# Kernel optimization log

Measured on AMD Instinct MI355X. Metric: run time of the kernel, lower is better.

## Reference

```python
import jax, jax.numpy as jnp
import numpy as np

QUERY_DIM = 512
INNER_DIM = 2 * QUERY_DIM  # 1024
CROSS_DIM = 512


def setup_inputs() -> dict:
    key = jax.random.key(0)
    k1, k2, k3, k4, k5, k6, k7 = jax.random.split(key, 7)
    B, N1, N2 = 8, 2048, 2048
    S1 = jax.random.normal(k1, (B, N1, CROSS_DIM), dtype=jnp.float32)
    S2 = jax.random.normal(k2, (B, N2, QUERY_DIM), dtype=jnp.float32)
    # Linear weights stored as [in, out] (pre-transposed vs torch's [out, in])
    sq = 1.0 / np.sqrt(QUERY_DIM)
    sc = 1.0 / np.sqrt(CROSS_DIM)
    si = 1.0 / np.sqrt(INNER_DIM)
    Wq = jax.random.uniform(k3, (QUERY_DIM, INNER_DIM), jnp.float32, -sq, sq)
    Wk = jax.random.uniform(k4, (CROSS_DIM, INNER_DIM), jnp.float32, -sc, sc)
    Wv = jax.random.uniform(k5, (CROSS_DIM, INNER_DIM), jnp.float32, -sc, sc)
    Wo = jax.random.uniform(k6, (INNER_DIM, QUERY_DIM), jnp.float32, -si, si)
    bo = jax.random.uniform(k7, (QUERY_DIM,), jnp.float32, -si, si)
    return {"S1": S1, "S2": S2, "Wq": Wq, "Wk": Wk, "Wv": Wv, "Wo": Wo, "bo": bo}


def reference(S1, S2, Wq, Wk, Wv, Wo, bo):
    # softmax((Wq S2)(Wk S1)^T) (Wv S1), then output projection. NOTE: no 1/sqrt(d) scaling.
    query = jnp.einsum('bnd,de->bne', S2, Wq)   # [B, N2, inner]
    key_ = jnp.einsum('bmd,de->bme', S1, Wk)    # [B, N1, inner]
    value = jnp.einsum('bmd,de->bme', S1, Wv)   # [B, N1, inner]
    scores = jnp.einsum('bne,bme->bnm', query, key_)  # [B, N2, N1]
    attn = jax.nn.softmax(scores, axis=-1)
    masked = jnp.einsum('bnm,bme->bne', attn, value)  # [B, N2, inner]
    out = jnp.einsum('bne,ed->bnd', masked, Wo) + bo  # [B, N2, query_dim]
    return out
```

## Files before the change

kernel.cpp:

```cpp
#include <hip/hip_runtime.h>


typedef _Float16 h_t;
typedef _Float16 h8 __attribute__((ext_vector_type(8)));
typedef _Float16 h4 __attribute__((ext_vector_type(4)));
typedef float f4 __attribute__((ext_vector_type(4)));

#define MFMA16(a, b, c) __builtin_amdgcn_mfma_f32_16x16x32_f16(a, b, c, 0, 0, 0)

typedef const __attribute__((address_space(1))) void* gas_t;
typedef __attribute__((address_space(3))) void* las_t;

__device__ __forceinline__ void gl2lds16(const void* g, void* l) {
    __builtin_amdgcn_global_load_lds((gas_t)g, (las_t)l, 16, 0, 0);
}

__global__ __launch_bounds__(256) void k_cast5(const float* __restrict__ S1,
                                               const float* __restrict__ S2,
                                               const float* __restrict__ Wq,
                                               const float* __restrict__ Wk,
                                               const float* __restrict__ Wv,
                                               h_t* __restrict__ S1h,
                                               h_t* __restrict__ S2h,
                                               h_t* __restrict__ Wqh,
                                               h_t* __restrict__ Wkh,
                                               h_t* __restrict__ Wvh) {
    long i = (long)blockIdx.x * 256 + threadIdx.x;
    const long n = 2097152;
    const long wn = 131072;
    const float* src;
    h_t* dst;
    long off;
    if (i < n) { src = S1; dst = S1h; off = i; }
    else if (i < 2 * n) { src = S2; dst = S2h; off = i - n; }
    else if (i < 2 * n + wn) { src = Wq; dst = Wqh; off = i - 2 * n; }
    else if (i < 2 * n + 2 * wn) { src = Wk; dst = Wkh; off = i - 2 * n - wn; }
    else { src = Wv; dst = Wvh; off = i - 2 * n - 2 * wn; }
    float4 v = *((const float4*)src + off);
    h4 h = {(h_t)v.x, (h_t)v.y, (h_t)v.z, (h_t)v.w};
    *((h4*)dst + off) = h;
}

__global__ __launch_bounds__(256) void k_transpose_o(const float* __restrict__ Wo,
                                                     h_t* __restrict__ Wot) {
    const int K = 1024, N = 512;
    int kb = blockIdx.y * 32, nb = blockIdx.x * 32;
    __shared__ float tile[32][33];
    int x = threadIdx.x & 31, y = threadIdx.x >> 5;
#pragma unroll
    for (int j = 0; j < 4; j++)
        tile[y + j * 8][x] = Wo[(size_t)(kb + y + j * 8) * N + nb + x];
    __syncthreads();
#pragma unroll
    for (int j = 0; j < 4; j++)
        Wot[(size_t)(nb + y + j * 8) * K + kb + x] = (h_t)tile[x][y + j * 8];
}

__global__ __launch_bounds__(256) void k_wpre(const h_t* __restrict__ Wqh,
                                              const h_t* __restrict__ Wkh,
                                              const h_t* __restrict__ Wot,
                                              const h_t* __restrict__ Wvh,
                                              h_t* __restrict__ Wkq,
                                              h_t* __restrict__ Wvot) {
    __shared__ h_t As[128 * 64];
    __shared__ h_t Bs[128 * 64];
    int t = threadIdx.x, w = t >> 6, lane = t & 63;
    int q16 = lane >> 4, l16 = lane & 15;
    int id = blockIdx.x;
    const h_t* A;
    const h_t* Bt;
    h_t* C;
    float oscale;
    if (id < 16) { A = Wkh; Bt = Wqh; C = Wkq; oscale = 1.44269504f; }
    else { id -= 16; A = Wot; Bt = Wvh; C = Wvot; oscale = 1.0f; }
    size_t m0 = (size_t)(id >> 2) * 128, n0 = (size_t)(id & 3) * 128;
    const int K = 1024, N = 512;
    int wr = (w >> 1) * 64, wc = (w & 1) * 64;
    f4 acc[4][4] = {};

    for (int k0 = 0; k0 < K; k0 += 64) {
#pragma unroll
        for (int j = 0; j < 4; j++) {
            int q = w * 4 + j;
            int row = q * 8 + (lane >> 3);
            int ks = (((lane & 7) ^ (row & 7)) << 3);
            gl2lds16(A + (m0 + row) * K + k0 + ks, &As[q * 512]);
            gl2lds16(Bt + (n0 + row) * K + k0 + ks, &Bs[q * 512]);
        }
        __syncthreads();
#pragma unroll
        for (int ks = 0; ks < 2; ks++) {
            h8 av[4], bv[4];
#pragma unroll
            for (int i = 0; i < 4; i++) {
                int row = wr + i * 16 + l16;
                int ch = ks * 4 + q16;
                av[i] = *(const h8*)&As[row * 64 + ((ch ^ (row & 7)) << 3)];
            }
#pragma unroll
            for (int j = 0; j < 4; j++) {
                int row = wc + j * 16 + l16;
                int ch = ks * 4 + q16;
                bv[j] = *(const h8*)&Bs[row * 64 + ((ch ^ (row & 7)) << 3)];
            }
#pragma unroll
            for (int i = 0; i < 4; i++)
#pragma unroll
                for (int j = 0; j < 4; j++)
                    acc[i][j] = MFMA16(av[i], bv[j], acc[i][j]);
        }
        __syncthreads();
    }
#pragma unroll
    for (int i = 0; i < 4; i++) {
        size_t r0 = m0 + wr + i * 16 + q16 * 4;
#pragma unroll
        for (int j = 0; j < 4; j++) {
            size_t c = n0 + wc + j * 16 + l16;
#pragma unroll
            for (int r = 0; r < 4; r++)
                C[(r0 + r) * N + c] = (h_t)(acc[i][j][r] * oscale);
        }
    }
}

__global__ __launch_bounds__(256) void k_proj2(const h_t* __restrict__ S2h,
                                               const h_t* __restrict__ S1h,
                                               const h_t* __restrict__ Wkq,
                                               const h_t* __restrict__ Wvot,
                                               const float* __restrict__ bo,
                                               h_t* __restrict__ T,
                                               h_t* __restrict__ Vt) {
    __shared__ h_t As[128 * 64];
    __shared__ h_t Bs[128 * 64];
    int t = threadIdx.x, w = t >> 6, lane = t & 63;
    int q16 = lane >> 4, l16 = lane & 15;
    int id = blockIdx.x;
    int mode = id >> 9;
    id &= 511;
    const h_t* A = mode ? S1h : S2h;
    const h_t* Bt = mode ? Wvot : Wkq;
    size_t m0 = (size_t)(id >> 2) * 128, n0 = (size_t)(id & 3) * 128;
    const int K = 512;
    int wr = (w >> 1) * 64, wc = (w & 1) * 64;
    f4 acc[4][4] = {};

    for (int k0 = 0; k0 < K; k0 += 64) {
#pragma unroll
        for (int j = 0; j < 4; j++) {
            int q = w * 4 + j;
            int row = q * 8 + (lane >> 3);
            int ks = (((lane & 7) ^ (row & 7)) << 3);
            gl2lds16(A + (m0 + row) * K + k0 + ks, &As[q * 512]);
            gl2lds16(Bt + (n0 + row) * K + k0 + ks, &Bs[q * 512]);
        }
        __syncthreads();
#pragma unroll
        for (int ks = 0; ks < 2; ks++) {
            h8 av[4], bv[4];
#pragma unroll
            for (int i = 0; i < 4; i++) {
                int row = wr + i * 16 + l16;
                int ch = ks * 4 + q16;
                av[i] = *(const h8*)&As[row * 64 + ((ch ^ (row & 7)) << 3)];
            }
#pragma unroll
            for (int j = 0; j < 4; j++) {
                int row = wc + j * 16 + l16;
                int ch = ks * 4 + q16;
                bv[j] = *(const h8*)&Bs[row * 64 + ((ch ^ (row & 7)) << 3)];
            }
#pragma unroll
            for (int i = 0; i < 4; i++)
#pragma unroll
                for (int j = 0; j < 4; j++)
                    acc[i][j] = MFMA16(av[i], bv[j], acc[i][j]);
        }
        __syncthreads();
    }
    if (mode == 0) {
#pragma unroll
        for (int i = 0; i < 4; i++) {
            size_t r0 = m0 + wr + i * 16 + q16 * 4;
#pragma unroll
            for (int j = 0; j < 4; j++) {
                size_t c = n0 + wc + j * 16 + l16;
#pragma unroll
                for (int r = 0; r < 4; r++)
                    T[(r0 + r) * 512 + c] = (h_t)acc[i][j][r];
            }
        }
    } else {
#pragma unroll
        for (int i = 0; i < 4; i++) {
            size_t gm = m0 + wr + i * 16 + q16 * 4;
            size_t b = gm >> 11;
            size_t n = gm & 2047;
#pragma unroll
            for (int j = 0; j < 4; j++) {
                size_t d = n0 + wc + j * 16 + l16;
                float bias = bo[d];
                h4 hv = {(h_t)(acc[i][j][0] + bias), (h_t)(acc[i][j][1] + bias),
                         (h_t)(acc[i][j][2] + bias), (h_t)(acc[i][j][3] + bias)};
                *(h4*)&Vt[(b * 512 + d) * 2048 + n] = hv;
            }
        }
    }
}

__global__ __launch_bounds__(256) void k_qk(const h_t* __restrict__ T,
                                            const h_t* __restrict__ S1h,
                                            h_t* __restrict__ P,
                                            float2* __restrict__ Mkt) {
    __shared__ h_t sm[18432];
    h_t* As = sm;
    h_t* Bs = sm + 8192;
    float* pmx = (float*)(sm + 17408);
    float* psm = (float*)(sm + 17920);
    int t = threadIdx.x, w = t >> 6, lane = t & 63;
    int q16 = lane >> 4, l16 = lane & 15;
    int qt = blockIdx.x, kt = blockIdx.y, b = blockIdx.z;
    const h_t* A = S1h + ((size_t)b * 2048 + kt * 128) * 512;
    const h_t* Bt = T + ((size_t)b * 2048 + qt * 128) * 512;
    int wr = (w >> 1) * 64, wc = (w & 1) * 64;
    f4 acc[4][4] = {};

    for (int k0 = 0; k0 < 512; k0 += 64) {
#pragma unroll
        for (int j = 0; j < 4; j++) {
            int q = w * 4 + j;
            int row = q * 8 + (lane >> 3);
            int ks = (((lane & 7) ^ (row & 7)) << 3);
            gl2lds16(A + (size_t)row * 512 + k0 + ks, &As[q * 512]);
            gl2lds16(Bt + (size_t)row * 512 + k0 + ks, &Bs[q * 512]);
        }
        __syncthreads();
#pragma unroll
        for (int ks = 0; ks < 2; ks++) {
            h8 av[4], bv[4];
#pragma unroll
            for (int i = 0; i < 4; i++) {
                int row = wr + i * 16 + l16;
                int ch = ks * 4 + q16;
                av[i] = *(const h8*)&As[row * 64 + ((ch ^ (row & 7)) << 3)];
            }
#pragma unroll
            for (int j = 0; j < 4; j++) {
                int row = wc + j * 16 + l16;
                int ch = ks * 4 + q16;
                bv[j] = *(const h8*)&Bs[row * 64 + ((ch ^ (row & 7)) << 3)];
            }
#pragma unroll
            for (int i = 0; i < 4; i++)
#pragma unroll
                for (int j = 0; j < 4; j++)
                    acc[i][j] = MFMA16(av[i], bv[j], acc[i][j]);
        }
        __syncthreads();
    }
    float lm[4], ls[4], sc[4];
#pragma unroll
    for (int j = 0; j < 4; j++) {
        float m = acc[0][j][0];
#pragma unroll
        for (int i = 0; i < 4; i++)
#pragma unroll
            for (int r = 0; r < 4; r++) m = fmaxf(m, acc[i][j][r]);
        lm[j] = m;
    }
#pragma unroll
    for (int msk = 16; msk <= 32; msk <<= 1)
#pragma unroll
        for (int j = 0; j < 4; j++)
            lm[j] = fmaxf(lm[j], __shfl_xor(lm[j], msk, 64));
#pragma unroll
    for (int j = 0; j < 4; j++) {
        float s = 0.f;
#pragma unroll
        for (int i = 0; i < 4; i++)
#pragma unroll
            for (int r = 0; r < 4; r++) {
                float e = exp2f(acc[i][j][r] - lm[j]);
                acc[i][j][r] = e;
                s += e;
            }
        ls[j] = s;
    }
#pragma unroll
    for (int msk = 16; msk <= 32; msk <<= 1)
#pragma unroll
        for (int j = 0; j < 4; j++) ls[j] += __shfl_xor(ls[j], msk, 64);
    if (q16 == 0) {
#pragma unroll
        for (int j = 0; j < 4; j++) {
            pmx[(w >> 1) * 128 + wc + j * 16 + l16] = lm[j];
            psm[(w >> 1) * 128 + wc + j * 16 + l16] = ls[j];
        }
    }
    __syncthreads();
#pragma unroll
    for (int j = 0; j < 4; j++) {
        int row = wc + j * 16 + l16;
        float om = pmx[((w >> 1) ^ 1) * 128 + row];
        float os = psm[((w >> 1) ^ 1) * 128 + row];
        float M = fmaxf(lm[j], om);
        float s = exp2f(lm[j] - M);
        float L = ls[j] * s + os * exp2f(om - M);
        sc[j] = s;
        if ((w >> 1) == 0 && q16 == 0)
            Mkt[((size_t)b * 16 + kt) * 2048 + qt * 128 + row] = make_float2(M, L);
    }
#pragma unroll
    for (int j = 0; j < 4; j++)
#pragma unroll
        for (int i = 0; i < 4; i++) {
            h4 hv = {(h_t)(acc[i][j][0] * sc[j]), (h_t)(acc[i][j][1] * sc[j]),
                     (h_t)(acc[i][j][2] * sc[j]), (h_t)(acc[i][j][3] * sc[j])};
            *(h4*)&sm[(wc + j * 16 + l16) * 136 + wr + i * 16 + q16 * 4] = hv;
        }
    __syncthreads();
    size_t Pbase = ((size_t)b * 2048 + qt * 128) * 2048 + (size_t)kt * 128;
#pragma unroll
    for (int p = 0; p < 8; p++) {
        int row = p * 16 + (t >> 4);
        int c8 = (t & 15) * 8;
        *(h8*)(P + Pbase + (size_t)row * 2048 + c8) = *(const h8*)&sm[row * 136 + c8];
    }
}

__global__ __launch_bounds__(256) void k_stats(const float2* __restrict__ Mkt,
                                               float2* __restrict__ MF,
                                               h_t* __restrict__ Dkt) {
    int r = blockIdx.x * 256 + threadIdx.x;
    int b = r >> 11, rowl = r & 2047;
    float2 v[16];
    float m = -1e30f;
#pragma unroll
    for (int kt = 0; kt < 16; kt++) {
        v[kt] = Mkt[((size_t)b * 16 + kt) * 2048 + rowl];
        m = fmaxf(m, v[kt].x);
    }
    float l = 0.f;
#pragma unroll
    for (int kt = 0; kt < 16; kt++) {
        float d = exp2f(v[kt].x - m);
        l += v[kt].y * d;
        Dkt[((size_t)b * 16 + kt) * 2048 + rowl] = (h_t)d;
    }
    MF[(size_t)b * 2048 + rowl] = make_float2(m, 1.f / l);
}

__global__ __launch_bounds__(256) void k_pv(const h_t* __restrict__ P,
                                            const h_t* __restrict__ Vt,
                                            const h_t* __restrict__ Dkt,
                                            const float2* __restrict__ MF,
                                            float* __restrict__ Out) {
    __shared__ h_t As[64 * 64];
    __shared__ h_t Bs[128 * 64];
    int t = threadIdx.x, w = t >> 6, lane = t & 63;
    int q16 = lane >> 4, l16 = lane & 15;
    int rt = blockIdx.x, dt = blockIdx.y, b = blockIdx.z;
    int rg = w >> 1, dg = w & 1;
    int sr = t >> 3, sc = t & 7;
    const h_t* Pb = P + ((size_t)b * 2048 + rt * 64) * 2048;
    const h_t* Vb = Vt + ((size_t)b * 512 + dt * 128) * 2048;
    f4 acc[2][4] = {};

    for (int kt = 0; kt < 16; kt++) {
        h_t d0 = Dkt[((size_t)b * 16 + kt) * 2048 + rt * 64 + sr];
        h_t d1 = Dkt[((size_t)b * 16 + kt) * 2048 + rt * 64 + 32 + sr];
#pragma unroll
        for (int h = 0; h < 2; h++) {
            int k0 = kt * 128 + h * 64;
#pragma unroll
            for (int p = 0; p < 2; p++) {
                int r_ = p * 32 + sr;
                h_t dh = p ? d1 : d0;
                h8 dv = {dh, dh, dh, dh, dh, dh, dh, dh};
                h8 v = *(const h8*)(Pb + (size_t)r_ * 2048 + k0 + sc * 8);
                v = v * dv;
                *(h8*)&As[r_ * 64 + ((sc ^ (r_ & 7)) << 3)] = v;
            }
#pragma unroll
            for (int j = 0; j < 4; j++) {
                int q = w * 4 + j;
                int row = q * 8 + (lane >> 3);
                int ks = (((lane & 7) ^ (row & 7)) << 3);
                gl2lds16(Vb + (size_t)row * 2048 + k0 + ks, &Bs[q * 512]);
            }
            __syncthreads();
#pragma unroll
            for (int ks = 0; ks < 2; ks++) {
                int ch = ks * 4 + q16;
                h8 av[2], bv[4];
#pragma unroll
                for (int i = 0; i < 2; i++) {
                    int row = rg * 32 + i * 16 + l16;
                    av[i] = *(const h8*)&As[row * 64 + ((ch ^ (row & 7)) << 3)];
                }
#pragma unroll
                for (int j = 0; j < 4; j++) {
                    int dr = dg * 64 + j * 16 + l16;
                    bv[j] = *(const h8*)&Bs[dr * 64 + ((ch ^ (dr & 7)) << 3)];
                }
#pragma unroll
                for (int i = 0; i < 2; i++)
#pragma unroll
                    for (int j = 0; j < 4; j++)
                        acc[i][j] = MFMA16(av[i], bv[j], acc[i][j]);
            }
            __syncthreads();
        }
    }
#pragma unroll
    for (int i = 0; i < 2; i++)
#pragma unroll
        for (int rr = 0; rr < 4; rr++) {
            int row = rg * 32 + i * 16 + q16 * 4 + rr;
            float linv = MF[(size_t)b * 2048 + rt * 64 + row].y;
#pragma unroll
            for (int j = 0; j < 4; j++) {
                int d = dt * 128 + dg * 64 + j * 16 + l16;
                Out[((size_t)b * 2048 + rt * 64 + row) * 512 + d] =
                    acc[i][j][rr] * linv;
            }
        }
}

extern "C" void kernel_launch(void* const* d_in, const int* in_sizes, int n_in,
                              void* d_out, int out_size, void* d_ws, size_t ws_size,
                              hipStream_t stream) {
    const float* S1 = (const float*)d_in[0];
    const float* S2 = (const float*)d_in[1];
    const float* Wq = (const float*)d_in[2];
    const float* Wk = (const float*)d_in[3];
    const float* Wv = (const float*)d_in[4];
    const float* Wo = (const float*)d_in[5];
    const float* bo = (const float*)d_in[6];
    float* Out = (float*)d_out;

    char* ws = (char*)d_ws;
    h_t* S1h  = (h_t*)(ws);
    h_t* T    = (h_t*)(ws + 16777216);
    h_t* Vt   = (h_t*)(ws + 33554432);
    h_t* P    = (h_t*)(ws + 50331648);
    float2* Mkt = (float2*)(ws + 117440512);
    h_t* S2h  = (h_t*)(ws + 50331648);
    h_t* Wqh  = (h_t*)(ws + 67108864);
    h_t* Wkh  = (h_t*)(ws + 68157440);
    h_t* Wvh  = (h_t*)(ws + 69206016);
    h_t* Wot  = (h_t*)(ws + 70254592);
    h_t* Wkq  = (h_t*)(ws + 71303168);
    h_t* Wvot = (h_t*)(ws + 71827456);
    h_t* Dkt  = (h_t*)(ws);
    float2* MF = (float2*)(ws + 524288);

    k_cast5<<<17920, 256, 0, stream>>>(S1, S2, Wq, Wk, Wv, S1h, S2h, Wqh, Wkh, Wvh);
    k_transpose_o<<<dim3(16, 32), 256, 0, stream>>>(Wo, Wot);
    k_wpre<<<32, 256, 0, stream>>>(Wqh, Wkh, Wot, Wvh, Wkq, Wvot);
    k_proj2<<<1024, 256, 0, stream>>>(S2h, S1h, Wkq, Wvot, bo, T, Vt);
    k_qk<<<dim3(16, 16, 8), 256, 0, stream>>>(T, S1h, P, Mkt);
    k_stats<<<64, 256, 0, stream>>>(Mkt, MF, Dkt);
    k_pv<<<dim3(32, 4, 8), 256, 0, stream>>>(P, Vt, Dkt, MF, Out);
}
```

Baseline: 284.5 us.

## Fuse softmax stats into PV kernel, merge prep kernels, enlarge PV row tile

Merges the fp16 cast kernel and the Wo transpose kernel into one launch. Folds the per-row softmax statistics computation into the PV kernel, so each block computes max and normalizer for its rows in shared memory, and drops the separate stats kernel with its Dkt and MF buffers. The PV tile grows from 64 to 128 rows per block, halving re-reads of V across row tiles and cutting the grid from 1024 to 512 blocks. In exchange each block recomputes the stats redundantly across the four d-tiles, holds more accumulators, and the grid may fill the GPU less well.

```diff
diff --git a/kernel.cpp b/kernel.cpp
--- a/kernel.cpp
+++ b/kernel.cpp
@@ -15,45 +15,48 @@
     __builtin_amdgcn_global_load_lds((gas_t)g, (las_t)l, 16, 0, 0);
 }
 
-__global__ __launch_bounds__(256) void k_cast5(const float* __restrict__ S1,
-                                               const float* __restrict__ S2,
-                                               const float* __restrict__ Wq,
-                                               const float* __restrict__ Wk,
-                                               const float* __restrict__ Wv,
-                                               h_t* __restrict__ S1h,
-                                               h_t* __restrict__ S2h,
-                                               h_t* __restrict__ Wqh,
-                                               h_t* __restrict__ Wkh,
-                                               h_t* __restrict__ Wvh) {
-    long i = (long)blockIdx.x * 256 + threadIdx.x;
-    const long n = 2097152;
-    const long wn = 131072;
-    const float* src;
-    h_t* dst;
-    long off;
-    if (i < n) { src = S1; dst = S1h; off = i; }
-    else if (i < 2 * n) { src = S2; dst = S2h; off = i - n; }
-    else if (i < 2 * n + wn) { src = Wq; dst = Wqh; off = i - 2 * n; }
-    else if (i < 2 * n + 2 * wn) { src = Wk; dst = Wkh; off = i - 2 * n - wn; }
-    else { src = Wv; dst = Wvh; off = i - 2 * n - 2 * wn; }
-    float4 v = *((const float4*)src + off);
-    h4 h = {(h_t)v.x, (h_t)v.y, (h_t)v.z, (h_t)v.w};
-    *((h4*)dst + off) = h;
-}
-
-__global__ __launch_bounds__(256) void k_transpose_o(const float* __restrict__ Wo,
-                                                     h_t* __restrict__ Wot) {
-    const int K = 1024, N = 512;
-    int kb = blockIdx.y * 32, nb = blockIdx.x * 32;
+__global__ __launch_bounds__(256) void k_prep(const float* __restrict__ S1,
+                                              const float* __restrict__ S2,
+                                              const float* __restrict__ Wq,
+                                              const float* __restrict__ Wk,
+                                              const float* __restrict__ Wv,
+                                              const float* __restrict__ Wo,
+                                              h_t* __restrict__ S1h,
+                                              h_t* __restrict__ S2h,
+                                              h_t* __restrict__ Wqh,
+                                              h_t* __restrict__ Wkh,
+                                              h_t* __restrict__ Wvh,
+                                              h_t* __restrict__ Wot) {
     __shared__ float tile[32][33];
-    int x = threadIdx.x & 31, y = threadIdx.x >> 5;
-#pragma unroll
-    for (int j = 0; j < 4; j++)
-        tile[y + j * 8][x] = Wo[(size_t)(kb + y + j * 8) * N + nb + x];
-    __syncthreads();
-#pragma unroll
-    for (int j = 0; j < 4; j++)
-        Wot[(size_t)(nb + y + j * 8) * K + kb + x] = (h_t)tile[x][y + j * 8];
+    long bid = blockIdx.x;
+    if (bid < 17920) {
+        long i = bid * 256 + threadIdx.x;
+        const long n = 2097152;
+        const long wn = 131072;
+        const float* src;
+        h_t* dst;
+        long off;
+        if (i < n) { src = S1; dst = S1h; off = i; }
+        else if (i < 2 * n) { src = S2; dst = S2h; off = i - n; }
+        else if (i < 2 * n + wn) { src = Wq; dst = Wqh; off = i - 2 * n; }
+        else if (i < 2 * n + 2 * wn) { src = Wk; dst = Wkh; off = i - 2 * n - wn; }
+        else { src = Wv; dst = Wvh; off = i - 2 * n - 2 * wn; }
+        float4 v = *((const float4*)src + off);
+        h4 h = {(h_t)v.x, (h_t)v.y, (h_t)v.z, (h_t)v.w};
+        *((h4*)dst + off) = h;
+    } else {
+        int tid = (int)(bid - 17920);
+        const int K = 1024, N = 512;
+        int nb = (tid & 15) * 32, kb = (tid >> 4) * 32;
+        int x = threadIdx.x & 31, y = threadIdx.x >> 5;
+#pragma unroll
+        for (int j = 0; j < 4; j++)
+            tile[y + j * 8][x] = Wo[(size_t)(kb + y + j * 8) * N + nb + x];
+        __syncthreads();
+#pragma unroll
+        for (int j = 0; j < 4; j++)
+            Wot[(size_t)(nb + y + j * 8) * K + kb + x] = (h_t)tile[x][y + j * 8];
+    }
 }
 
 __global__ __launch_bounds__(256) void k_wpre(const h_t* __restrict__ Wqh,
@@ -328,101 +331,94 @@
     }
 }
 
-__global__ __launch_bounds__(256) void k_stats(const float2* __restrict__ Mkt,
-                                               float2* __restrict__ MF,
-                                               h_t* __restrict__ Dkt) {
-    int r = blockIdx.x * 256 + threadIdx.x;
-    int b = r >> 11, rowl = r & 2047;
-    float2 v[16];
-    float m = -1e30f;
-#pragma unroll
-    for (int kt = 0; kt < 16; kt++) {
-        v[kt] = Mkt[((size_t)b * 16 + kt) * 2048 + rowl];
-        m = fmaxf(m, v[kt].x);
-    }
-    float l = 0.f;
-#pragma unroll
-    for (int kt = 0; kt < 16; kt++) {
-        float d = exp2f(v[kt].x - m);
-        l += v[kt].y * d;
-        Dkt[((size_t)b * 16 + kt) * 2048 + rowl] = (h_t)d;
-    }
-    MF[(size_t)b * 2048 + rowl] = make_float2(m, 1.f / l);
-}
-
 __global__ __launch_bounds__(256) void k_pv(const h_t* __restrict__ P,
                                             const h_t* __restrict__ Vt,
-                                            const h_t* __restrict__ Dkt,
-                                            const float2* __restrict__ MF,
+                                            const float2* __restrict__ Mkt,
                                             float* __restrict__ Out) {
-    __shared__ h_t As[64 * 64];
+    __shared__ h_t As[128 * 64];
     __shared__ h_t Bs[128 * 64];
+    __shared__ h_t dks[16][128];
+    __shared__ float linv[128];
     int t = threadIdx.x, w = t >> 6, lane = t & 63;
     int q16 = lane >> 4, l16 = lane & 15;
     int rt = blockIdx.x, dt = blockIdx.y, b = blockIdx.z;
     int rg = w >> 1, dg = w & 1;
-    int sr = t >> 3, sc = t & 7;
-    const h_t* Pb = P + ((size_t)b * 2048 + rt * 64) * 2048;
+    if (t < 128) {
+        float2 v[16];
+        float m = -1e30f;
+#pragma unroll
+        for (int kt = 0; kt < 16; kt++) {
+            v[kt] = Mkt[((size_t)b * 16 + kt) * 2048 + rt * 128 + t];
+            m = fmaxf(m, v[kt].x);
+        }
+        float l = 0.f;
+#pragma unroll
+        for (int kt = 0; kt < 16; kt++) {
+            float d = exp2f(v[kt].x - m);
+            l += v[kt].y * d;
+            dks[kt][t] = (h_t)d;
+        }
+        linv[t] = 1.f / l;
+    }
+    __syncthreads();
+
+    const h_t* Pb = P + ((size_t)b * 2048 + rt * 128) * 2048;
     const h_t* Vb = Vt + ((size_t)b * 512 + dt * 128) * 2048;
-    f4 acc[2][4] = {};
-
-    for (int kt = 0; kt < 16; kt++) {
-        h_t d0 = Dkt[((size_t)b * 16 + kt) * 2048 + rt * 64 + sr];
-        h_t d1 = Dkt[((size_t)b * 16 + kt) * 2048 + rt * 64 + 32 + sr];
-#pragma unroll
-        for (int h = 0; h < 2; h++) {
-            int k0 = kt * 128 + h * 64;
-#pragma unroll
-            for (int p = 0; p < 2; p++) {
-                int r_ = p * 32 + sr;
-                h_t dh = p ? d1 : d0;
-                h8 dv = {dh, dh, dh, dh, dh, dh, dh, dh};
-                h8 v = *(const h8*)(Pb + (size_t)r_ * 2048 + k0 + sc * 8);
-                v = v * dv;
-                *(h8*)&As[r_ * 64 + ((sc ^ (r_ & 7)) << 3)] = v;
-            }
-#pragma unroll
-            for (int j = 0; j < 4; j++) {
-                int q = w * 4 + j;
-                int row = q * 8 + (lane >> 3);
-                int ks = (((lane & 7) ^ (row & 7)) << 3);
-                gl2lds16(Vb + (size_t)row * 2048 + k0 + ks, &Bs[q * 512]);
-            }
-            __syncthreads();
-#pragma unroll
-            for (int ks = 0; ks < 2; ks++) {
-                int ch = ks * 4 + q16;
-                h8 av[2], bv[4];
-#pragma unroll
-                for (int i = 0; i < 2; i++) {
-                    int row = rg * 32 + i * 16 + l16;
-                    av[i] = *(const h8*)&As[row * 64 + ((ch ^ (row & 7)) << 3)];
-                }
-#pragma unroll
-                for (int j = 0; j < 4; j++) {
-                    int dr = dg * 64 + j * 16 + l16;
-                    bv[j] = *(const h8*)&Bs[dr * 64 + ((ch ^ (dr & 7)) << 3)];
-                }
-#pragma unroll
-                for (int i = 0; i < 2; i++)
-#pragma unroll
-                    for (int j = 0; j < 4; j++)
-                        acc[i][j] = MFMA16(av[i], bv[j], acc[i][j]);
-            }
-            __syncthreads();
-        }
-    }
-#pragma unroll
-    for (int i = 0; i < 2; i++)
+    int srow = t >> 3, soct = t & 7;
+    f4 acc[4][4] = {};
+
+    for (int k0 = 0; k0 < 2048; k0 += 64) {
+        int kt = k0 >> 7;
+#pragma unroll
+        for (int p = 0; p < 4; p++) {
+            int r_ = p * 32 + srow;
+            h_t dh = dks[kt][r_];
+            h8 dv = {dh, dh, dh, dh, dh, dh, dh, dh};
+            h8 v = *(const h8*)(Pb + (size_t)r_ * 2048 + k0 + soct * 8);
+            v = v * dv;
+            *(h8*)&As[r_ * 64 + ((soct ^ (r_ & 7)) << 3)] = v;
+        }
+#pragma unroll
+        for (int j = 0; j < 4; j++) {
+            int q = w * 4 + j;
+            int row = q * 8 + (lane >> 3);
+            int ks = (((lane & 7) ^ (row & 7)) << 3);
+            gl2lds16(Vb + (size_t)row * 2048 + k0 + ks, &Bs[q * 512]);
+        }
+        __syncthreads();
+#pragma unroll
+        for (int ks = 0; ks < 2; ks++) {
+            int ch = ks * 4 + q16;
+            h8 av[4], bv[4];
+#pragma unroll
+            for (int i = 0; i < 4; i++) {
+                int row = rg * 64 + i * 16 + l16;
+                av[i] = *(const h8*)&As[row * 64 + ((ch ^ (row & 7)) << 3)];
+            }
+#pragma unroll
+            for (int j = 0; j < 4; j++) {
+                int dr = dg * 64 + j * 16 + l16;
+                bv[j] = *(const h8*)&Bs[dr * 64 + ((ch ^ (dr & 7)) << 3)];
+            }
+#pragma unroll
+            for (int i = 0; i < 4; i++)
+#pragma unroll
+                for (int j = 0; j < 4; j++)
+                    acc[i][j] = MFMA16(av[i], bv[j], acc[i][j]);
+        }
+        __syncthreads();
+    }
+#pragma unroll
+    for (int i = 0; i < 4; i++)
 #pragma unroll
         for (int rr = 0; rr < 4; rr++) {
-            int row = rg * 32 + i * 16 + q16 * 4 + rr;
-            float linv = MF[(size_t)b * 2048 + rt * 64 + row].y;
+            int row = rg * 64 + i * 16 + q16 * 4 + rr;
+            float lv = linv[row];
 #pragma unroll
             for (int j = 0; j < 4; j++) {
                 int d = dt * 128 + dg * 64 + j * 16 + l16;
-                Out[((size_t)b * 2048 + rt * 64 + row) * 512 + d] =
-                    acc[i][j][rr] * linv;
+                Out[((size_t)b * 2048 + rt * 128 + row) * 512 + d] =
+                    acc[i][j][rr] * lv;
             }
         }
 }
@@ -452,14 +448,11 @@
     h_t* Wot  = (h_t*)(ws + 70254592);
     h_t* Wkq  = (h_t*)(ws + 71303168);
     h_t* Wvot = (h_t*)(ws + 71827456);
-    h_t* Dkt  = (h_t*)(ws);
-    float2* MF = (float2*)(ws + 524288);
-
-    k_cast5<<<17920, 256, 0, stream>>>(S1, S2, Wq, Wk, Wv, S1h, S2h, Wqh, Wkh, Wvh);
-    k_transpose_o<<<dim3(16, 32), 256, 0, stream>>>(Wo, Wot);
+
+    k_prep<<<18432, 256, 0, stream>>>(S1, S2, Wq, Wk, Wv, Wo,
+                                      S1h, S2h, Wqh, Wkh, Wvh, Wot);
     k_wpre<<<32, 256, 0, stream>>>(Wqh, Wkh, Wot, Wvh, Wkq, Wvot);
     k_proj2<<<1024, 256, 0, stream>>>(S2h, S1h, Wkq, Wvot, bo, T, Vt);
     k_qk<<<dim3(16, 16, 8), 256, 0, stream>>>(T, S1h, P, Mkt);
-    k_stats<<<64, 256, 0, stream>>>(Mkt, MF, Dkt);
-    k_pv<<<dim3(32, 4, 8), 256, 0, stream>>>(P, Vt, Dkt, MF, Out);
-}
+    k_pv<<<dim3(16, 4, 8), 256, 0, stream>>>(P, Vt, Mkt, Out);
+}
```

Measured after the change: 280.4 us. Within noise of the previous version (-1.5%).
